# Performance work log

Hardware: AMD Instinct MI355X
Metric: run time of the kernel (lower is better)

Reference implementation:

```python
import jax, jax.numpy as jnp
import numpy as np

N = 50000          # num nodes
E = 800000         # num edges (before self-loops)
F_IN = 128
H = 4              # heads
C1 = 16            # hidden channels per head
C2 = 8             # out channels per head
NEG_SLOPE = 0.2
EPS = 1e-16


def setup_inputs() -> dict:
    key = jax.random.key(0)
    ks = jax.random.split(key, 10)
    x = jax.random.normal(ks[0], (N, F_IN), dtype=jnp.float32)
    edge_index = jax.random.randint(ks[1], (2, E), 0, N, dtype=jnp.int64)
    s1 = 1.0 / np.sqrt(F_IN)
    s2 = 1.0 / np.sqrt(H * C1)
    return {
        "x": x,
        "edge_index": edge_index,
        "W1": jax.random.normal(ks[2], (F_IN, H * C1), dtype=jnp.float32) * s1,
        "a_src1": jax.random.normal(ks[3], (H, C1), dtype=jnp.float32) * s2,
        "a_dst1": jax.random.normal(ks[4], (H, C1), dtype=jnp.float32) * s2,
        "b1": jnp.zeros((H * C1,), dtype=jnp.float32),
        "W2": jax.random.normal(ks[5], (H * C1, H * C2), dtype=jnp.float32) * s2,
        "a_src2": jax.random.normal(ks[6], (H, C2), dtype=jnp.float32) * 0.2,
        "a_dst2": jax.random.normal(ks[7], (H, C2), dtype=jnp.float32) * 0.2,
        "b2": jnp.zeros((H * C2,), dtype=jnp.float32),
    }


def _gat_conv(x, src, dst, W, a_src, a_dst, b, heads, ch):
    # linear transform -> per-head features [N, H, C]
    h = (x @ W).reshape(-1, heads, ch)
    # per-node attention logits [N, H]
    al_src = jnp.sum(h * a_src[None], axis=-1)
    al_dst = jnp.sum(h * a_dst[None], axis=-1)
    # edge-wise logits + leaky relu [E, H]
    e = al_src[src] + al_dst[dst]
    e = jnp.where(e >= 0, e, NEG_SLOPE * e)
    # segment softmax over destination neighborhoods
    m = jax.ops.segment_max(e, dst, num_segments=N)
    e = jnp.exp(e - m[dst])
    s = jax.ops.segment_sum(e, dst, num_segments=N)
    alpha = e / (s[dst] + EPS)                      # [E, H]
    # weighted gather-scatter aggregate [N, H, C]
    msg = h[src] * alpha[..., None]
    out = jax.ops.segment_sum(msg, dst, num_segments=N)
    # concat heads + bias
    return out.reshape(-1, heads * ch) + b


def reference(x, edge_index, W1, a_src1, a_dst1, b1, W2, a_src2, a_dst2, b2):
    # PyG GATConv adds self-loops by default
    loop = jnp.arange(N, dtype=edge_index.dtype)
    src = jnp.concatenate([edge_index[0], loop])
    dst = jnp.concatenate([edge_index[1], loop])
    h = _gat_conv(x, src, dst, W1, a_src1, a_dst1, b1, H, C1)
    h = jax.nn.relu(h)
    h = _gat_conv(h, src, dst, W2, a_src2, a_dst2, b2, H, C2)
    return jax.nn.log_softmax(h, axis=1)
```

## Files before the change

kernel.cpp:

```cpp
#include <hip/hip_runtime.h>
#include <hip/hip_bf16.h>
#include <math.h>

#define NN 50000
#define NE 800000
#define ET (NE + NN)
#define DCAP 128
#define SG 196
#define ECH 8192
#define NCH 104
#define NPASS 8
#define NRANGE 6250

__device__ __forceinline__ float bf2f(unsigned short u) {
    return __uint_as_float(((unsigned)u) << 16);
}
__device__ __forceinline__ unsigned short f2bf(float f) {
    unsigned u = __float_as_uint(f);
    return (unsigned short)((u + 0x7fff + ((u >> 16) & 1)) >> 16);
}
__device__ __forceinline__ float lrelu(float e) {
    return e >= 0.f ? e : 0.2f * e;
}

__global__ __launch_bounds__(1024) void k_prep(const unsigned long long* __restrict__ ei,
                                               const unsigned int* __restrict__ x,
                                               int* __restrict__ iflag, int* __restrict__ fflag) {
    int b = blockIdx.x, t = threadIdx.x;
    if (b == 0) {
        __shared__ int any;
        if (t == 0) any = 0;
        __syncthreads();
        if (ei[t] >= (unsigned long long)NN) atomicOr(&any, 1);
        __syncthreads();
        if (t == 0) *iflag = any ? 0 : 1;
    } else {
        __shared__ int cnt[16];
        unsigned w = x[t];
        unsigned e = (w >> 7) & 0xFFu;
        int c = (e >= 96 && e <= 140) ? 1 : 0;
        #pragma unroll
        for (int off = 32; off; off >>= 1) c += __shfl_xor(c, off);
        if ((t & 63) == 0) cnt[t >> 6] = c;
        __syncthreads();
        if (t == 0) {
            int s = 0;
            #pragma unroll
            for (int q = 0; q < 16; q++) s += cnt[q];
            *fflag = (s > 700) ? 1 : 0;
        }
    }
}

__global__ void k_convert_hist(const void* __restrict__ raw,
                               const void* p2, const void* p3, const void* p4, const void* p5,
                               const void* p6, const void* p7, const void* p8, const void* p9,
                               const int* __restrict__ iflag, const int* __restrict__ fflag,
                               int2* __restrict__ pairs,
                               int* __restrict__ deg, float* __restrict__ wsm) {
    int e = blockIdx.x * 256 + threadIdx.x;
    if (e < 10528) {
        const void* p; int off;
        if (e < 8192)       { p = p2; off = e; }
        else if (e < 8256)  { p = p3; off = e - 8192; }
        else if (e < 8320)  { p = p4; off = e - 8256; }
        else if (e < 8384)  { p = p5; off = e - 8320; }
        else if (e < 10432) { p = p6; off = e - 8384; }
        else if (e < 10464) { p = p7; off = e - 10432; }
        else if (e < 10496) { p = p8; off = e - 10464; }
        else                { p = p9; off = e - 10496; }
        wsm[e] = (*fflag) ? bf2f(((const unsigned short*)p)[off]) : ((const float*)p)[off];
    }
    if (e >= ET) return;
    int s, d;
    if (e >= NE) { s = d = e - NE; }
    else if (*iflag) {
        s = (int)((const long long*)raw)[e];
        d = (int)((const long long*)raw)[NE + e];
    } else {
        s = ((const int*)raw)[e];
        d = ((const int*)raw)[NE + e];
    }
    pairs[e] = make_int2(s, d);
    atomicAdd(&deg[d], 1);
}

__device__ __forceinline__ int block_excl_scan(int v, int* lds, int t) {
    int lane = t & 63, wid = t >> 6;
    int inc = v;
    #pragma unroll
    for (int d = 1; d < 64; d <<= 1) {
        int u = __shfl_up(inc, d);
        if (lane >= d) inc += u;
    }
    if (lane == 63) lds[wid] = inc;
    __syncthreads();
    if (t == 0) {
        int a = lds[0], b = lds[1], c = lds[2];
        lds[4] = 0; lds[5] = a; lds[6] = a + b; lds[7] = a + b + c;
    }
    __syncthreads();
    return lds[4 + wid] + inc - v;
}

__global__ __launch_bounds__(256) void k_scan_up(const int* __restrict__ deg, int* __restrict__ bsum) {
    __shared__ int lds[8];
    int t = threadIdx.x, i = blockIdx.x * 256 + t;
    int v = (i < NN) ? deg[i] : 0;
    #pragma unroll
    for (int off = 32; off; off >>= 1) v += __shfl_xor(v, off);
    if ((t & 63) == 0) lds[t >> 6] = v;
    __syncthreads();
    if (t == 0) bsum[blockIdx.x] = lds[0] + lds[1] + lds[2] + lds[3];
}

__global__ __launch_bounds__(256) void k_scan_mid(const int* __restrict__ bsum, int* __restrict__ boff) {
    __shared__ int lds[8];
    int t = threadIdx.x;
    int v = (t < SG) ? bsum[t] : 0;
    int e = block_excl_scan(v, lds, t);
    if (t < SG) boff[t] = e;
}

__global__ __launch_bounds__(256) void k_scan_down(const int* __restrict__ deg, const int* __restrict__ boff,
                                                   int* __restrict__ rs, int* __restrict__ cur) {
    __shared__ int lds[8];
    int t = threadIdx.x, i = blockIdx.x * 256 + t;
    int v = (i < NN) ? deg[i] : 0;
    int e = block_excl_scan(v, lds, t) + boff[blockIdx.x];
    if (i < NN) {
        rs[i] = e; cur[i] = e;
        if (i == NN - 1) rs[NN] = e + v;
    }
}

__global__ __launch_bounds__(256) void k_scatter8(const int2* __restrict__ pairs,
                                                  int* __restrict__ cur, int* __restrict__ csr) {
    int b = blockIdx.x;
    int pass = b & (NPASS - 1);
    int chunk = b >> 3;
    int lo = pass * NRANGE, hi = lo + NRANGE;
    int base = chunk * ECH;
    for (int i = threadIdx.x; i < ECH; i += 256) {
        int e = base + i;
        if (e < ET) {
            int2 pr = pairs[e];
            if (pr.y >= lo && pr.y < hi) {
                int pos = atomicAdd(&cur[pr.y], 1);
                csr[pos] = pr.x;
            }
        }
    }
}

__global__ __launch_bounds__(256) void k_gemm1(const void* __restrict__ xraw,
                                               const void* __restrict__ w1raw,
                                               const void* __restrict__ as1raw,
                                               const void* __restrict__ ad1raw,
                                               const int* __restrict__ fflag,
                                               unsigned short* __restrict__ h1b,
                                               float* __restrict__ als, float* __restrict__ ald) {
    __shared__ unsigned int Wp[64 * 65];
    __shared__ float xt[32 * 132];
    int tid = threadIdx.x;
    int rb = blockIdx.x * 32;
    int fl = *fflag;
    for (int i = tid; i < 64 * 64; i += 256) {
        int k2 = i >> 6, c = i & 63;
        unsigned lo, hi;
        if (fl) {
            lo = ((const unsigned short*)w1raw)[(2 * k2) * 64 + c];
            hi = ((const unsigned short*)w1raw)[(2 * k2 + 1) * 64 + c];
        } else {
            lo = f2bf(((const float*)w1raw)[(2 * k2) * 64 + c]);
            hi = f2bf(((const float*)w1raw)[(2 * k2 + 1) * 64 + c]);
        }
        Wp[c * 65 + k2] = lo | (hi << 16);
    }
    if (fl) {
        const unsigned short* xb = (const unsigned short*)xraw;
        for (int i = tid; i < 32 * 16; i += 256) {
            int r = i >> 4, k8 = i & 15;
            float f[8];
            if (rb + r < NN) {
                uint4 v = ((const uint4*)xb)[(size_t)(rb + r) * 16 + k8];
                f[0] = bf2f((unsigned short)(v.x & 0xffff)); f[1] = bf2f((unsigned short)(v.x >> 16));
                f[2] = bf2f((unsigned short)(v.y & 0xffff)); f[3] = bf2f((unsigned short)(v.y >> 16));
                f[4] = bf2f((unsigned short)(v.z & 0xffff)); f[5] = bf2f((unsigned short)(v.z >> 16));
                f[6] = bf2f((unsigned short)(v.w & 0xffff)); f[7] = bf2f((unsigned short)(v.w >> 16));
            } else {
                #pragma unroll
                for (int q = 0; q < 8; q++) f[q] = 0.f;
            }
            int o = r * 132 + k8 * 8;
            *(float4*)&xt[o]     = make_float4(f[0], f[1], f[2], f[3]);
            *(float4*)&xt[o + 4] = make_float4(f[4], f[5], f[6], f[7]);
        }
    } else {
        const float* xf = (const float*)xraw;
        for (int i = tid; i < 32 * 32; i += 256) {
            int r = i >> 5, kq = i & 31;
            float4 v = make_float4(0.f, 0.f, 0.f, 0.f);
            if (rb + r < NN) v = ((const float4*)xf)[(size_t)(rb + r) * 32 + kq];
            *(float4*)&xt[r * 132 + kq * 4] = v;
        }
    }
    __syncthreads();
    int c = tid & 63;
    int rg = tid >> 6;
    float acc[8];
    #pragma unroll
    for (int j = 0; j < 8; j++) acc[j] = 0.f;
    for (int k2 = 0; k2 < 64; k2 += 2) {
        unsigned p0 = Wp[c * 65 + k2];
        unsigned p1 = Wp[c * 65 + k2 + 1];
        float w0 = __uint_as_float(p0 << 16);
        float w1 = __uint_as_float(p0 & 0xffff0000u);
        float w2 = __uint_as_float(p1 << 16);
        float w3 = __uint_as_float(p1 & 0xffff0000u);
        int kk = k2 * 2;
        #pragma unroll
        for (int j = 0; j < 8; j++) {
            float4 xv = *(const float4*)&xt[(rg * 8 + j) * 132 + kk];
            acc[j] = fmaf(xv.x, w0, fmaf(xv.y, w1, fmaf(xv.z, w2, fmaf(xv.w, w3, acc[j]))));
        }
    }
    float asf = fl ? bf2f(((const unsigned short*)as1raw)[c]) : ((const float*)as1raw)[c];
    float adf = fl ? bf2f(((const unsigned short*)ad1raw)[c]) : ((const float*)ad1raw)[c];
    #pragma unroll
    for (int j = 0; j < 8; j++) {
        int r = rb + rg * 8 + j;
        bool ok = r < NN;
        if (ok) h1b[(size_t)r * 64 + c] = f2bf(acc[j]);
        float v = acc[j] * asf, w = acc[j] * adf;
        #pragma unroll
        for (int off = 1; off < 16; off <<= 1) {
            v += __shfl_xor(v, off);
            w += __shfl_xor(w, off);
        }
        if (ok && (c & 15) == 0) {
            als[r * 4 + (c >> 4)] = v;
            ald[r * 4 + (c >> 4)] = w;
        }
    }
}

__global__ __launch_bounds__(256) void k_gemm2(const float* __restrict__ in,
                                               const float* __restrict__ Wf,
                                               const float* __restrict__ asf_p,
                                               const float* __restrict__ adf_p,
                                               unsigned short* __restrict__ h2b,
                                               float* __restrict__ als, float* __restrict__ ald) {
    __shared__ float Wt[32 * 65];
    __shared__ float xt[64 * 68];
    int tid = threadIdx.x;
    int rb = blockIdx.x * 64;
    for (int i = tid; i < 64 * 32; i += 256) {
        int k = i >> 5, c = i & 31;
        Wt[c * 65 + k] = Wf[i];
    }
    for (int i = tid; i < 64 * 16; i += 256) {
        int r = i >> 4, kq = i & 15;
        float4 v = make_float4(0.f, 0.f, 0.f, 0.f);
        if (rb + r < NN) v = ((const float4*)in)[(size_t)(rb + r) * 16 + kq];
        *(float4*)&xt[r * 68 + kq * 4] = v;
    }
    __syncthreads();
    int c = tid & 31, rg = tid >> 5;
    float acc[8];
    #pragma unroll
    for (int j = 0; j < 8; j++) acc[j] = 0.f;
    #pragma unroll 2
    for (int k = 0; k < 64; k += 4) {
        float4 w;
        w.x = Wt[c * 65 + k];     w.y = Wt[c * 65 + k + 1];
        w.z = Wt[c * 65 + k + 2]; w.w = Wt[c * 65 + k + 3];
        #pragma unroll
        for (int j = 0; j < 8; j++) {
            float4 xv = *(const float4*)&xt[(rg * 8 + j) * 68 + k];
            acc[j] = fmaf(xv.x, w.x, fmaf(xv.y, w.y, fmaf(xv.z, w.z, fmaf(xv.w, w.w, acc[j]))));
        }
    }
    float asf = asf_p[c], adf = adf_p[c];
    #pragma unroll
    for (int j = 0; j < 8; j++) {
        int r = rb + rg * 8 + j;
        bool ok = r < NN;
        if (ok) h2b[(size_t)r * 32 + c] = f2bf(acc[j]);
        float v = acc[j] * asf, w = acc[j] * adf;
        #pragma unroll
        for (int off = 1; off < 8; off <<= 1) {
            v += __shfl_xor(v, off);
            w += __shfl_xor(w, off);
        }
        if (ok && (c & 7) == 0) {
            als[r * 4 + (c >> 3)] = v;
            ald[r * 4 + (c >> 3)] = w;
        }
    }
}

__global__ __launch_bounds__(256) void k_agg1(const int* __restrict__ rs, const int* __restrict__ csr,
                                              const float* __restrict__ als, const float* __restrict__ aldv,
                                              const unsigned short* __restrict__ h1b,
                                              const float* __restrict__ b1,
                                              float* __restrict__ out1) {
    __shared__ float pv[4][DCAP * 4];
    __shared__ int  sidx[4][DCAP];
    int w = threadIdx.x >> 6, lane = threadIdx.x & 63;
    int n = blockIdx.x * 4 + w;
    if (n >= NN) return;
    int base = rs[n];
    int deg = rs[n + 1] - base;
    float4 ald = *(const float4*)(aldv + 4 * n);

    if (deg <= DCAP) {
        int sA = 0;
        bool v0 = lane < deg, v1 = lane + 64 < deg;
        if (v0) {
            sA = csr[base + lane];
            sidx[w][lane] = sA;
            float4 a = *(const float4*)(als + 4 * sA);
            float4 p;
            p.x = __expf(lrelu(a.x + ald.x)); p.y = __expf(lrelu(a.y + ald.y));
            p.z = __expf(lrelu(a.z + ald.z)); p.w = __expf(lrelu(a.w + ald.w));
            *(float4*)&pv[w][lane * 4] = p;
        }
        if (v1) {
            int sB = csr[base + lane + 64];
            sidx[w][lane + 64] = sB;
            float4 a = *(const float4*)(als + 4 * sB);
            float4 p;
            p.x = __expf(lrelu(a.x + ald.x)); p.y = __expf(lrelu(a.y + ald.y));
            p.z = __expf(lrelu(a.z + ald.z)); p.w = __expf(lrelu(a.w + ald.w));
            *(float4*)&pv[w][(lane + 64) * 4] = p;
        }
        int degp = (deg + 3) & ~3;
        int s0v = __shfl(sA, 0);
        if (lane >= deg && lane < degp) {
            sidx[w][lane] = s0v;
            *(float4*)&pv[w][lane * 4] = make_float4(0.f, 0.f, 0.f, 0.f);
        }
        int i1 = lane + 64;
        if (i1 >= deg && i1 < degp) {
            sidx[w][i1] = s0v;
            *(float4*)&pv[w][i1 * 4] = make_float4(0.f, 0.f, 0.f, 0.f);
        }
        int g = lane >> 4, j = lane & 15, hh = j >> 2;
        float4 a4 = make_float4(0.f, 0.f, 0.f, 0.f);
        float ps = 0.f;
        for (int e = 0; e < degp; e += 4) {
            int s = sidx[w][e + g];
            float ph = pv[w][(e + g) * 4 + hh];
            uint2 rv = *(const uint2*)&h1b[(size_t)s * 64 + j * 4];
            ps += ph;
            a4.x = fmaf(ph, bf2f((unsigned short)(rv.x & 0xffff)), a4.x);
            a4.y = fmaf(ph, bf2f((unsigned short)(rv.x >> 16)),    a4.y);
            a4.z = fmaf(ph, bf2f((unsigned short)(rv.y & 0xffff)), a4.z);
            a4.w = fmaf(ph, bf2f((unsigned short)(rv.y >> 16)),    a4.w);
        }
        #pragma unroll
        for (int off = 16; off <= 32; off <<= 1) {
            a4.x += __shfl_xor(a4.x, off);
            a4.y += __shfl_xor(a4.y, off);
            a4.z += __shfl_xor(a4.z, off);
            a4.w += __shfl_xor(a4.w, off);
            ps   += __shfl_xor(ps,   off);
        }
        if (g == 0) {
            float rh = 1.f / (ps + 1e-16f);
            float4 bb = *(const float4*)&b1[j * 4];
            float4 o;
            o.x = fmaxf(a4.x * rh + bb.x, 0.f);
            o.y = fmaxf(a4.y * rh + bb.y, 0.f);
            o.z = fmaxf(a4.z * rh + bb.z, 0.f);
            o.w = fmaxf(a4.w * rh + bb.w, 0.f);
            *(float4*)&out1[(size_t)n * 64 + j * 4] = o;
        }
    } else {
        int h = lane >> 4;
        float s0 = 0.f, s1 = 0.f, s2 = 0.f, s3 = 0.f;
        for (int i = lane; i < deg; i += 64) {
            int s = csr[base + i];
            float4 a = *(const float4*)(als + 4 * s);
            s0 += __expf(lrelu(a.x + ald.x));
            s1 += __expf(lrelu(a.y + ald.y));
            s2 += __expf(lrelu(a.z + ald.z));
            s3 += __expf(lrelu(a.w + ald.w));
        }
        #pragma unroll
        for (int off = 32; off; off >>= 1) {
            s0 += __shfl_xor(s0, off);
            s1 += __shfl_xor(s1, off);
            s2 += __shfl_xor(s2, off);
            s3 += __shfl_xor(s3, off);
        }
        float sh = (h == 0) ? s0 : (h == 1) ? s1 : (h == 2) ? s2 : s3;
        float ah = (h == 0) ? ald.x : (h == 1) ? ald.y : (h == 2) ? ald.z : ald.w;
        float rh = 1.f / (sh + 1e-16f);
        float acc = 0.f;
        for (int e = 0; e < deg; ++e) {
            int s = csr[base + e];
            float av = als[4 * s + h];
            float ph = __expf(lrelu(av + ah));
            acc = fmaf(ph, bf2f(h1b[(size_t)s * 64 + lane]), acc);
        }
        out1[(size_t)n * 64 + lane] = fmaxf(acc * rh + b1[lane], 0.f);
    }
}

__global__ __launch_bounds__(256) void k_agg2(const int* __restrict__ rs, const int* __restrict__ csr,
                                              const float* __restrict__ als, const float* __restrict__ aldv,
                                              const unsigned short* __restrict__ h2b,
                                              const float* __restrict__ b2,
                                              float* __restrict__ out) {
    __shared__ float pv[4][DCAP * 4];
    __shared__ int  sidx[4][DCAP];
    int w = threadIdx.x >> 6, lane = threadIdx.x & 63;
    int n = blockIdx.x * 4 + w;
    if (n >= NN) return;
    int base = rs[n];
    int deg = rs[n + 1] - base;
    float4 ald = *(const float4*)(aldv + 4 * n);

    if (deg <= DCAP) {
        int sA = 0;
        bool v0 = lane < deg, v1 = lane + 64 < deg;
        if (v0) {
            sA = csr[base + lane];
            sidx[w][lane] = sA;
            float4 a = *(const float4*)(als + 4 * sA);
            float4 p;
            p.x = __expf(lrelu(a.x + ald.x)); p.y = __expf(lrelu(a.y + ald.y));
            p.z = __expf(lrelu(a.z + ald.z)); p.w = __expf(lrelu(a.w + ald.w));
            *(float4*)&pv[w][lane * 4] = p;
        }
        if (v1) {
            int sB = csr[base + lane + 64];
            sidx[w][lane + 64] = sB;
            float4 a = *(const float4*)(als + 4 * sB);
            float4 p;
            p.x = __expf(lrelu(a.x + ald.x)); p.y = __expf(lrelu(a.y + ald.y));
            p.z = __expf(lrelu(a.z + ald.z)); p.w = __expf(lrelu(a.w + ald.w));
            *(float4*)&pv[w][(lane + 64) * 4] = p;
        }
        int degp = (deg + 7) & ~7;
        int s0v = __shfl(sA, 0);
        if (lane >= deg && lane < degp) {
            sidx[w][lane] = s0v;
            *(float4*)&pv[w][lane * 4] = make_float4(0.f, 0.f, 0.f, 0.f);
        }
        int i1 = lane + 64;
        if (i1 >= deg && i1 < degp) {
            sidx[w][i1] = s0v;
            *(float4*)&pv[w][i1 * 4] = make_float4(0.f, 0.f, 0.f, 0.f);
        }
        int g = lane >> 3, j = lane & 7, hh = j >> 1;
        float4 a4 = make_float4(0.f, 0.f, 0.f, 0.f);
        float ps = 0.f;
        for (int e = 0; e < degp; e += 8) {
            int s = sidx[w][e + g];
            float ph = pv[w][(e + g) * 4 + hh];
            uint2 rv = *(const uint2*)&h2b[(size_t)s * 32 + j * 4];
            ps += ph;
            a4.x = fmaf(ph, bf2f((unsigned short)(rv.x & 0xffff)), a4.x);
            a4.y = fmaf(ph, bf2f((unsigned short)(rv.x >> 16)),    a4.y);
            a4.z = fmaf(ph, bf2f((unsigned short)(rv.y & 0xffff)), a4.z);
            a4.w = fmaf(ph, bf2f((unsigned short)(rv.y >> 16)),    a4.w);
        }
        #pragma unroll
        for (int off = 8; off <= 32; off <<= 1) {
            a4.x += __shfl_xor(a4.x, off);
            a4.y += __shfl_xor(a4.y, off);
            a4.z += __shfl_xor(a4.z, off);
            a4.w += __shfl_xor(a4.w, off);
            ps   += __shfl_xor(ps,   off);
        }
        float rh = 1.f / (ps + 1e-16f);
        float4 bb = *(const float4*)&b2[j * 4];
        float4 row;
        row.x = a4.x * rh + bb.x; row.y = a4.y * rh + bb.y;
        row.z = a4.z * rh + bb.z; row.w = a4.w * rh + bb.w;
        float mx = fmaxf(fmaxf(row.x, row.y), fmaxf(row.z, row.w));
        #pragma unroll
        for (int off = 1; off < 8; off <<= 1) mx = fmaxf(mx, __shfl_xor(mx, off));
        float sm = __expf(row.x - mx) + __expf(row.y - mx)
                 + __expf(row.z - mx) + __expf(row.w - mx);
        #pragma unroll
        for (int off = 1; off < 8; off <<= 1) sm += __shfl_xor(sm, off);
        float lse = mx + logf(sm);
        if (g == 0) {
            float4 o;
            o.x = row.x - lse; o.y = row.y - lse;
            o.z = row.z - lse; o.w = row.w - lse;
            *(float4*)&out[(size_t)n * 32 + j * 4] = o;
        }
    } else {
        float s0 = 0.f, s1 = 0.f, s2 = 0.f, s3 = 0.f;
        for (int i = lane; i < deg; i += 64) {
            int s = csr[base + i];
            float4 a = *(const float4*)(als + 4 * s);
            s0 += __expf(lrelu(a.x + ald.x));
            s1 += __expf(lrelu(a.y + ald.y));
            s2 += __expf(lrelu(a.z + ald.z));
            s3 += __expf(lrelu(a.w + ald.w));
        }
        #pragma unroll
        for (int off = 32; off; off >>= 1) {
            s0 += __shfl_xor(s0, off);
            s1 += __shfl_xor(s1, off);
            s2 += __shfl_xor(s2, off);
            s3 += __shfl_xor(s3, off);
        }
        int L = lane & 31;
        int h2i = L >> 3;
        float sh2 = (h2i == 0) ? s0 : (h2i == 1) ? s1 : (h2i == 2) ? s2 : s3;
        float ah2 = (h2i == 0) ? ald.x : (h2i == 1) ? ald.y : (h2i == 2) ? ald.z : ald.w;
        float rh2 = 1.f / (sh2 + 1e-16f);
        if (lane < 32) {
            float acc = 0.f;
            for (int e = 0; e < deg; ++e) {
                int s = csr[base + e];
                float av = als[4 * s + h2i];
                float ph = __expf(lrelu(av + ah2));
                acc = fmaf(ph, bf2f(h2b[(size_t)s * 32 + L]), acc);
            }
            float row = acc * rh2 + b2[L];
            float mx = row;
            #pragma unroll
            for (int off = 16; off; off >>= 1) mx = fmaxf(mx, __shfl_xor(mx, off, 32));
            float pe = __expf(row - mx);
            float sm = pe;
            #pragma unroll
            for (int off = 16; off; off >>= 1) sm += __shfl_xor(sm, off, 32);
            out[(size_t)n * 32 + L] = row - mx - logf(sm);
        }
    }
}

extern "C" void kernel_launch(void* const* d_in, const int* in_sizes, int n_in,
                              void* d_out, int out_size, void* d_ws, size_t ws_size,
                              hipStream_t stream) {
    const void* x  = d_in[0];
    const void* ei = d_in[1];
    float* out = (float*)d_out;

    char* p = (char*)d_ws;
    auto take = [&](size_t b) -> char* {
        char* r = p; p += (b + 255) & ~(size_t)255; return r;
    };
    int*   iflag = (int*)take(sizeof(int));
    int*   fflag = (int*)take(sizeof(int));
    int*   deg   = (int*)take(sizeof(int) * NN);
    int*   rs    = (int*)take(sizeof(int) * (NN + 1));
    int*   cur   = (int*)take(sizeof(int) * NN);
    int*   bsum  = (int*)take(sizeof(int) * 256);
    int*   boff  = (int*)take(sizeof(int) * 256);
    int2*  pairs = (int2*)take(sizeof(int2) * ET);
    int*   csr   = (int*)take(sizeof(int) * ET);
    float* wsm   = (float*)take(sizeof(float) * 10528);
    unsigned short* h1b = (unsigned short*)take(sizeof(unsigned short) * (size_t)NN * 64);
    float* als1  = (float*)take(sizeof(float) * NN * 4);
    float* ald1  = (float*)take(sizeof(float) * NN * 4);
    float* out1  = (float*)take(sizeof(float) * (size_t)NN * 64);
    unsigned short* h2b = (unsigned short*)take(sizeof(unsigned short) * (size_t)NN * 32);
    float* als2  = (float*)take(sizeof(float) * NN * 4);
    float* ald2  = (float*)take(sizeof(float) * NN * 4);

    float* Wf2  = wsm + 8384;
    float* as2f = wsm + 10432;
    float* ad2f = wsm + 10464;
    float* b1f  = wsm + 8320;
    float* b2f  = wsm + 10496;

    hipMemsetAsync(deg, 0, sizeof(int) * NN, stream);
    k_prep<<<2, 1024, 0, stream>>>((const unsigned long long*)ei, (const unsigned int*)x,
                                   iflag, fflag);
    k_convert_hist<<<(ET + 255) / 256, 256, 0, stream>>>(ei, d_in[2], d_in[3], d_in[4], d_in[5],
                                                         d_in[6], d_in[7], d_in[8], d_in[9],
                                                         iflag, fflag, pairs, deg, wsm);
    k_gemm1<<<(NN + 31) / 32, 256, 0, stream>>>(x, d_in[2], d_in[3], d_in[4], fflag,
                                                h1b, als1, ald1);
    k_scan_up<<<SG, 256, 0, stream>>>(deg, bsum);
    k_scan_mid<<<1, 256, 0, stream>>>(bsum, boff);
    k_scan_down<<<SG, 256, 0, stream>>>(deg, boff, rs, cur);
    k_scatter8<<<NPASS * NCH, 256, 0, stream>>>(pairs, cur, csr);

    k_agg1<<<(NN + 3) / 4, 256, 0, stream>>>(rs, csr, als1, ald1, h1b, b1f, out1);

    k_gemm2<<<(NN + 63) / 64, 256, 0, stream>>>(out1, Wf2, as2f, ad2f, h2b, als2, ald2);
    k_agg2<<<(NN + 3) / 4, 256, 0, stream>>>(rs, csr, als2, ald2, h2b, b2f, out);
}
```

Baseline: 273.9 us.

## Fuse prep, convert/histogram and gemm1 into one kernel; single-pass decoupled scan

Merges the flag-detection kernel, the edge convert/degree-histogram kernel and the first GEMM into one launch. Every block recomputes the dtype flags locally, and blocks are interleaved between histogram and GEMM roles. It also replaces the three-kernel scan with a single kernel where blocks publish partial sums and spin on an atomic counter. This cuts launch count and idle gaps, at the cost of redundant flag reads per block and a spin-wait that relies on all 196 blocks being co-resident.

```diff
diff --git a/kernel.cpp b/kernel.cpp
--- a/kernel.cpp
+++ b/kernel.cpp
@@ -12,6 +12,11 @@
 #define NPASS 8
 #define NRANGE 6250
 
+#define NCV 3321
+#define NG1 1563
+#define SPLITB (3 * NG1)
+#define TOTB (NCV + NG1)
+
 __device__ __forceinline__ float bf2f(unsigned short u) {
     return __uint_as_float(((unsigned)u) << 16);
 }
@@ -23,66 +28,154 @@
     return e >= 0.f ? e : 0.2f * e;
 }
 
-__global__ __launch_bounds__(1024) void k_prep(const unsigned long long* __restrict__ ei,
-                                               const unsigned int* __restrict__ x,
-                                               int* __restrict__ iflag, int* __restrict__ fflag) {
-    int b = blockIdx.x, t = threadIdx.x;
-    if (b == 0) {
-        __shared__ int any;
-        if (t == 0) any = 0;
-        __syncthreads();
-        if (ei[t] >= (unsigned long long)NN) atomicOr(&any, 1);
-        __syncthreads();
-        if (t == 0) *iflag = any ? 0 : 1;
+__global__ __launch_bounds__(256) void k_front(const void* __restrict__ xraw,
+                                               const void* __restrict__ ei,
+                                               const void* p2, const void* p3, const void* p4, const void* p5,
+                                               const void* p6, const void* p7, const void* p8, const void* p9,
+                                               int2* __restrict__ pairs, int* __restrict__ deg,
+                                               float* __restrict__ wsm,
+                                               unsigned short* __restrict__ h1b,
+                                               float* __restrict__ als, float* __restrict__ ald) {
+    __shared__ unsigned int Wp[64 * 65];
+    __shared__ float xt[32 * 132];
+    __shared__ int wred[8];
+    int t = threadIdx.x;
+    int b = blockIdx.x;
+
+    const unsigned long long* e64 = (const unsigned long long*)ei;
+    const unsigned int* x32 = (const unsigned int*)xraw;
+    int ci = 0, cf = 0;
+    #pragma unroll
+    for (int q = 0; q < 4; q++) {
+        if (e64[4 * t + q] >= (unsigned long long)NN) ci = 1;
+        unsigned ex = (x32[4 * t + q] >> 7) & 0xFFu;
+        cf += (ex >= 96 && ex <= 140) ? 1 : 0;
+    }
+    #pragma unroll
+    for (int off = 32; off; off >>= 1) { ci |= __shfl_xor(ci, off); cf += __shfl_xor(cf, off); }
+    if ((t & 63) == 0) { wred[t >> 6] = ci; wred[4 + (t >> 6)] = cf; }
+    __syncthreads();
+    int iflag = (wred[0] | wred[1] | wred[2] | wred[3]) ? 0 : 1;
+    int fl = ((wred[4] + wred[5] + wred[6] + wred[7]) > 700) ? 1 : 0;
+
+    int role, id;
+    if (b < SPLITB) {
+        int g = b / 3, r = b % 3;
+        if (r == 2) { role = 1; id = g; }
+        else        { role = 0; id = 2 * g + r; }
     } else {
-        __shared__ int cnt[16];
-        unsigned w = x[t];
-        unsigned e = (w >> 7) & 0xFFu;
-        int c = (e >= 96 && e <= 140) ? 1 : 0;
-        #pragma unroll
-        for (int off = 32; off; off >>= 1) c += __shfl_xor(c, off);
-        if ((t & 63) == 0) cnt[t >> 6] = c;
-        __syncthreads();
-        if (t == 0) {
-            int s = 0;
-            #pragma unroll
-            for (int q = 0; q < 16; q++) s += cnt[q];
-            *fflag = (s > 700) ? 1 : 0;
-        }
-    }
-}
-
-__global__ void k_convert_hist(const void* __restrict__ raw,
-                               const void* p2, const void* p3, const void* p4, const void* p5,
-                               const void* p6, const void* p7, const void* p8, const void* p9,
-                               const int* __restrict__ iflag, const int* __restrict__ fflag,
-                               int2* __restrict__ pairs,
-                               int* __restrict__ deg, float* __restrict__ wsm) {
-    int e = blockIdx.x * 256 + threadIdx.x;
-    if (e < 10528) {
-        const void* p; int off;
-        if (e < 8192)       { p = p2; off = e; }
-        else if (e < 8256)  { p = p3; off = e - 8192; }
-        else if (e < 8320)  { p = p4; off = e - 8256; }
-        else if (e < 8384)  { p = p5; off = e - 8320; }
-        else if (e < 10432) { p = p6; off = e - 8384; }
-        else if (e < 10464) { p = p7; off = e - 10432; }
-        else if (e < 10496) { p = p8; off = e - 10464; }
-        else                { p = p9; off = e - 10496; }
-        wsm[e] = (*fflag) ? bf2f(((const unsigned short*)p)[off]) : ((const float*)p)[off];
-    }
-    if (e >= ET) return;
-    int s, d;
-    if (e >= NE) { s = d = e - NE; }
-    else if (*iflag) {
-        s = (int)((const long long*)raw)[e];
-        d = (int)((const long long*)raw)[NE + e];
+        role = 0; id = b - NG1;
+    }
+
+    if (role == 0) {
+        int e = id * 256 + t;
+        if (e < 10528) {
+            const void* p; int off;
+            if (e < 8192)       { p = p2; off = e; }
+            else if (e < 8256)  { p = p3; off = e - 8192; }
+            else if (e < 8320)  { p = p4; off = e - 8256; }
+            else if (e < 8384)  { p = p5; off = e - 8320; }
+            else if (e < 10432) { p = p6; off = e - 8384; }
+            else if (e < 10464) { p = p7; off = e - 10432; }
+            else if (e < 10496) { p = p8; off = e - 10464; }
+            else                { p = p9; off = e - 10496; }
+            wsm[e] = fl ? bf2f(((const unsigned short*)p)[off]) : ((const float*)p)[off];
+        }
+        if (e >= ET) return;
+        int s, d;
+        if (e >= NE) { s = d = e - NE; }
+        else if (iflag) {
+            s = (int)((const long long*)ei)[e];
+            d = (int)((const long long*)ei)[NE + e];
+        } else {
+            s = ((const int*)ei)[e];
+            d = ((const int*)ei)[NE + e];
+        }
+        pairs[e] = make_int2(s, d);
+        atomicAdd(&deg[d], 1);
+        return;
+    }
+
+    const void* w1raw = p2; const void* as1raw = p3; const void* ad1raw = p4;
+    int rb = id * 32;
+    for (int i = t; i < 64 * 64; i += 256) {
+        int k2 = i >> 6, c = i & 63;
+        unsigned lo, hi;
+        if (fl) {
+            lo = ((const unsigned short*)w1raw)[(2 * k2) * 64 + c];
+            hi = ((const unsigned short*)w1raw)[(2 * k2 + 1) * 64 + c];
+        } else {
+            lo = f2bf(((const float*)w1raw)[(2 * k2) * 64 + c]);
+            hi = f2bf(((const float*)w1raw)[(2 * k2 + 1) * 64 + c]);
+        }
+        Wp[c * 65 + k2] = lo | (hi << 16);
+    }
+    if (fl) {
+        const unsigned short* xb = (const unsigned short*)xraw;
+        for (int i = t; i < 32 * 16; i += 256) {
+            int r = i >> 4, k8 = i & 15;
+            float f[8];
+            if (rb + r < NN) {
+                uint4 v = ((const uint4*)xb)[(size_t)(rb + r) * 16 + k8];
+                f[0] = bf2f((unsigned short)(v.x & 0xffff)); f[1] = bf2f((unsigned short)(v.x >> 16));
+                f[2] = bf2f((unsigned short)(v.y & 0xffff)); f[3] = bf2f((unsigned short)(v.y >> 16));
+                f[4] = bf2f((unsigned short)(v.z & 0xffff)); f[5] = bf2f((unsigned short)(v.z >> 16));
+                f[6] = bf2f((unsigned short)(v.w & 0xffff)); f[7] = bf2f((unsigned short)(v.w >> 16));
+            } else {
+                #pragma unroll
+                for (int q = 0; q < 8; q++) f[q] = 0.f;
+            }
+            int o = r * 132 + k8 * 8;
+            *(float4*)&xt[o]     = make_float4(f[0], f[1], f[2], f[3]);
+            *(float4*)&xt[o + 4] = make_float4(f[4], f[5], f[6], f[7]);
+        }
     } else {
-        s = ((const int*)raw)[e];
-        d = ((const int*)raw)[NE + e];
-    }
-    pairs[e] = make_int2(s, d);
-    atomicAdd(&deg[d], 1);
+        const float* xf = (const float*)xraw;
+        for (int i = t; i < 32 * 32; i += 256) {
+            int r = i >> 5, kq = i & 31;
+            float4 v = make_float4(0.f, 0.f, 0.f, 0.f);
+            if (rb + r < NN) v = ((const float4*)xf)[(size_t)(rb + r) * 32 + kq];
+            *(float4*)&xt[r * 132 + kq * 4] = v;
+        }
+    }
+    __syncthreads();
+    int c = t & 63;
+    int rg = t >> 6;
+    float acc[8];
+    #pragma unroll
+    for (int j = 0; j < 8; j++) acc[j] = 0.f;
+    for (int k2 = 0; k2 < 64; k2 += 2) {
+        unsigned q0 = Wp[c * 65 + k2];
+        unsigned q1 = Wp[c * 65 + k2 + 1];
+        float w0 = __uint_as_float(q0 << 16);
+        float w1 = __uint_as_float(q0 & 0xffff0000u);
+        float w2 = __uint_as_float(q1 << 16);
+        float w3 = __uint_as_float(q1 & 0xffff0000u);
+        int kk = k2 * 2;
+        #pragma unroll
+        for (int j = 0; j < 8; j++) {
+            float4 xv = *(const float4*)&xt[(rg * 8 + j) * 132 + kk];
+            acc[j] = fmaf(xv.x, w0, fmaf(xv.y, w1, fmaf(xv.z, w2, fmaf(xv.w, w3, acc[j]))));
+        }
+    }
+    float asf = fl ? bf2f(((const unsigned short*)as1raw)[c]) : ((const float*)as1raw)[c];
+    float adf = fl ? bf2f(((const unsigned short*)ad1raw)[c]) : ((const float*)ad1raw)[c];
+    #pragma unroll
+    for (int j = 0; j < 8; j++) {
+        int r = rb + rg * 8 + j;
+        bool ok = r < NN;
+        if (ok) h1b[(size_t)r * 64 + c] = f2bf(acc[j]);
+        float v = acc[j] * asf, w = acc[j] * adf;
+        #pragma unroll
+        for (int off = 1; off < 16; off <<= 1) {
+            v += __shfl_xor(v, off);
+            w += __shfl_xor(w, off);
+        }
+        if (ok && (c & 15) == 0) {
+            als[r * 4 + (c >> 4)] = v;
+            ald[r * 4 + (c >> 4)] = w;
+        }
+    }
 }
 
 __device__ __forceinline__ int block_excl_scan(int v, int* lds, int t) {
@@ -103,34 +196,36 @@
     return lds[4 + wid] + inc - v;
 }
 
-__global__ __launch_bounds__(256) void k_scan_up(const int* __restrict__ deg, int* __restrict__ bsum) {
+__global__ __launch_bounds__(256) void k_scan(const int* __restrict__ deg, int* __restrict__ bsum,
+                                              int* __restrict__ ctr,
+                                              int* __restrict__ rs, int* __restrict__ cur) {
     __shared__ int lds[8];
-    int t = threadIdx.x, i = blockIdx.x * 256 + t;
+    __shared__ int sOff, sTot;
+    int t = threadIdx.x, b = blockIdx.x;
+    int i = b * 256 + t;
     int v = (i < NN) ? deg[i] : 0;
-    #pragma unroll
-    for (int off = 32; off; off >>= 1) v += __shfl_xor(v, off);
-    if ((t & 63) == 0) lds[t >> 6] = v;
-    __syncthreads();
-    if (t == 0) bsum[blockIdx.x] = lds[0] + lds[1] + lds[2] + lds[3];
-}
-
-__global__ __launch_bounds__(256) void k_scan_mid(const int* __restrict__ bsum, int* __restrict__ boff) {
-    __shared__ int lds[8];
-    int t = threadIdx.x;
-    int v = (t < SG) ? bsum[t] : 0;
-    int e = block_excl_scan(v, lds, t);
-    if (t < SG) boff[t] = e;
-}
-
-__global__ __launch_bounds__(256) void k_scan_down(const int* __restrict__ deg, const int* __restrict__ boff,
-                                                   int* __restrict__ rs, int* __restrict__ cur) {
-    __shared__ int lds[8];
-    int t = threadIdx.x, i = blockIdx.x * 256 + t;
-    int v = (i < NN) ? deg[i] : 0;
-    int e = block_excl_scan(v, lds, t) + boff[blockIdx.x];
+    int e_loc = block_excl_scan(v, lds, t);
+    if (t == 255) {
+        bsum[b] = e_loc + v;
+        __threadfence();
+        atomicAdd(ctr, 1);
+    }
+    if (t == 0) {
+        while (__hip_atomic_load(ctr, __ATOMIC_ACQUIRE, __HIP_MEMORY_SCOPE_AGENT) < SG) {
+            __builtin_amdgcn_s_sleep(1);
+        }
+    }
+    __syncthreads();
+    __threadfence();
+    int bv = (t < SG) ? bsum[t] : 0;
+    int be = block_excl_scan(bv, lds, t);
+    if (t == b) sOff = be;
+    if (t == SG - 1) sTot = be + bv;
+    __syncthreads();
+    int e = sOff + e_loc;
     if (i < NN) {
         rs[i] = e; cur[i] = e;
-        if (i == NN - 1) rs[NN] = e + v;
+        if (i == NN - 1) rs[NN] = sTot;
     }
 }
 
@@ -149,98 +244,6 @@
                 int pos = atomicAdd(&cur[pr.y], 1);
                 csr[pos] = pr.x;
             }
-        }
-    }
-}
-
-__global__ __launch_bounds__(256) void k_gemm1(const void* __restrict__ xraw,
-                                               const void* __restrict__ w1raw,
-                                               const void* __restrict__ as1raw,
-                                               const void* __restrict__ ad1raw,
-                                               const int* __restrict__ fflag,
-                                               unsigned short* __restrict__ h1b,
-                                               float* __restrict__ als, float* __restrict__ ald) {
-    __shared__ unsigned int Wp[64 * 65];
-    __shared__ float xt[32 * 132];
-    int tid = threadIdx.x;
-    int rb = blockIdx.x * 32;
-    int fl = *fflag;
-    for (int i = tid; i < 64 * 64; i += 256) {
-        int k2 = i >> 6, c = i & 63;
-        unsigned lo, hi;
-        if (fl) {
-            lo = ((const unsigned short*)w1raw)[(2 * k2) * 64 + c];
-            hi = ((const unsigned short*)w1raw)[(2 * k2 + 1) * 64 + c];
-        } else {
-            lo = f2bf(((const float*)w1raw)[(2 * k2) * 64 + c]);
-            hi = f2bf(((const float*)w1raw)[(2 * k2 + 1) * 64 + c]);
-        }
-        Wp[c * 65 + k2] = lo | (hi << 16);
-    }
-    if (fl) {
-        const unsigned short* xb = (const unsigned short*)xraw;
-        for (int i = tid; i < 32 * 16; i += 256) {
-            int r = i >> 4, k8 = i & 15;
-            float f[8];
-            if (rb + r < NN) {
-                uint4 v = ((const uint4*)xb)[(size_t)(rb + r) * 16 + k8];
-                f[0] = bf2f((unsigned short)(v.x & 0xffff)); f[1] = bf2f((unsigned short)(v.x >> 16));
-                f[2] = bf2f((unsigned short)(v.y & 0xffff)); f[3] = bf2f((unsigned short)(v.y >> 16));
-                f[4] = bf2f((unsigned short)(v.z & 0xffff)); f[5] = bf2f((unsigned short)(v.z >> 16));
-                f[6] = bf2f((unsigned short)(v.w & 0xffff)); f[7] = bf2f((unsigned short)(v.w >> 16));
-            } else {
-                #pragma unroll
-                for (int q = 0; q < 8; q++) f[q] = 0.f;
-            }
-            int o = r * 132 + k8 * 8;
-            *(float4*)&xt[o]     = make_float4(f[0], f[1], f[2], f[3]);
-            *(float4*)&xt[o + 4] = make_float4(f[4], f[5], f[6], f[7]);
-        }
-    } else {
-        const float* xf = (const float*)xraw;
-        for (int i = tid; i < 32 * 32; i += 256) {
-            int r = i >> 5, kq = i & 31;
-            float4 v = make_float4(0.f, 0.f, 0.f, 0.f);
-            if (rb + r < NN) v = ((const float4*)xf)[(size_t)(rb + r) * 32 + kq];
-            *(float4*)&xt[r * 132 + kq * 4] = v;
-        }
-    }
-    __syncthreads();
-    int c = tid & 63;
-    int rg = tid >> 6;
-    float acc[8];
-    #pragma unroll
-    for (int j = 0; j < 8; j++) acc[j] = 0.f;
-    for (int k2 = 0; k2 < 64; k2 += 2) {
-        unsigned p0 = Wp[c * 65 + k2];
-        unsigned p1 = Wp[c * 65 + k2 + 1];
-        float w0 = __uint_as_float(p0 << 16);
-        float w1 = __uint_as_float(p0 & 0xffff0000u);
-        float w2 = __uint_as_float(p1 << 16);
-        float w3 = __uint_as_float(p1 & 0xffff0000u);
-        int kk = k2 * 2;
-        #pragma unroll
-        for (int j = 0; j < 8; j++) {
-            float4 xv = *(const float4*)&xt[(rg * 8 + j) * 132 + kk];
-            acc[j] = fmaf(xv.x, w0, fmaf(xv.y, w1, fmaf(xv.z, w2, fmaf(xv.w, w3, acc[j]))));
-        }
-    }
-    float asf = fl ? bf2f(((const unsigned short*)as1raw)[c]) : ((const float*)as1raw)[c];
-    float adf = fl ? bf2f(((const unsigned short*)ad1raw)[c]) : ((const float*)ad1raw)[c];
-    #pragma unroll
-    for (int j = 0; j < 8; j++) {
-        int r = rb + rg * 8 + j;
-        bool ok = r < NN;
-        if (ok) h1b[(size_t)r * 64 + c] = f2bf(acc[j]);
-        float v = acc[j] * asf, w = acc[j] * adf;
-        #pragma unroll
-        for (int off = 1; off < 16; off <<= 1) {
-            v += __shfl_xor(v, off);
-            w += __shfl_xor(w, off);
-        }
-        if (ok && (c & 15) == 0) {
-            als[r * 4 + (c >> 4)] = v;
-            ald[r * 4 + (c >> 4)] = w;
         }
     }
 }
@@ -549,13 +552,12 @@
     auto take = [&](size_t b) -> char* {
         char* r = p; p += (b + 255) & ~(size_t)255; return r;
     };
-    int*   iflag = (int*)take(sizeof(int));
-    int*   fflag = (int*)take(sizeof(int));
-    int*   deg   = (int*)take(sizeof(int) * NN);
+    int*   degc  = (int*)take(sizeof(int) * (NN + 8));
+    int*   deg   = degc;
+    int*   ctr   = degc + NN;
     int*   rs    = (int*)take(sizeof(int) * (NN + 1));
     int*   cur   = (int*)take(sizeof(int) * NN);
     int*   bsum  = (int*)take(sizeof(int) * 256);
-    int*   boff  = (int*)take(sizeof(int) * 256);
     int2*  pairs = (int2*)take(sizeof(int2) * ET);
     int*   csr   = (int*)take(sizeof(int) * ET);
     float* wsm   = (float*)take(sizeof(float) * 10528);
@@ -573,17 +575,11 @@
     float* b1f  = wsm + 8320;
     float* b2f  = wsm + 10496;
 
-    hipMemsetAsync(deg, 0, sizeof(int) * NN, stream);
-    k_prep<<<2, 1024, 0, stream>>>((const unsigned long long*)ei, (const unsigned int*)x,
-                                   iflag, fflag);
-    k_convert_hist<<<(ET + 255) / 256, 256, 0, stream>>>(ei, d_in[2], d_in[3], d_in[4], d_in[5],
-                                                         d_in[6], d_in[7], d_in[8], d_in[9],
-                                                         iflag, fflag, pairs, deg, wsm);
-    k_gemm1<<<(NN + 31) / 32, 256, 0, stream>>>(x, d_in[2], d_in[3], d_in[4], fflag,
-                                                h1b, als1, ald1);
-    k_scan_up<<<SG, 256, 0, stream>>>(deg, bsum);
-    k_scan_mid<<<1, 256, 0, stream>>>(bsum, boff);
-    k_scan_down<<<SG, 256, 0, stream>>>(deg, boff, rs, cur);
+    hipMemsetAsync(degc, 0, sizeof(int) * (NN + 8), stream);
+    k_front<<<TOTB, 256, 0, stream>>>(x, ei, d_in[2], d_in[3], d_in[4], d_in[5],
+                                      d_in[6], d_in[7], d_in[8], d_in[9],
+                                      pairs, deg, wsm, h1b, als1, ald1);
+    k_scan<<<SG, 256, 0, stream>>>(deg, bsum, ctr, rs, cur);
     k_scatter8<<<NPASS * NCH, 256, 0, stream>>>(pairs, cur, csr);
 
     k_agg1<<<(NN + 3) / 4, 256, 0, stream>>>(rs, csr, als1, ald1, h1b, b1f, out1);
```

New measurement: 276.2 us. No clear change (+0.9%).
